# Kernel tuning notes

Hardware: AMD Instinct MI355X
Metric: run time of the kernel (lower is better)

The kernel has to match this reference:

```python
import jax, jax.numpy as jnp
import numpy as np

B, T, D_IN, H, NUM_LAYERS = 64, 512, 512, 500, 2


def _lstm_dir(x, mask, W_ih, W_hh, b, reverse):
    """One unidirectional LSTM over padded batch. x:[B,T,D], mask:[B,T,1] bool.
    AllenNLP AugmentedLstm gate order: input, forget, memory(cell), output."""
    bsz = x.shape[0]
    h_dim = W_hh.shape[1]
    # Precompute all input-side gate projections in one big GEMM: [B,T,4H]
    x_gates = jnp.einsum('btd,gd->btg', x, W_ih) + b

    def step(carry, inp):
        h, c = carry
        gx, m = inp  # gx:[B,4H], m:[B,1]
        gates = gx + h @ W_hh.T
        i, f, g, o = jnp.split(gates, 4, axis=-1)
        i = jax.nn.sigmoid(i)
        f = jax.nn.sigmoid(f)
        g = jnp.tanh(g)
        o = jax.nn.sigmoid(o)
        c_new = f * c + i * g
        h_new = o * jnp.tanh(c_new)
        h = jnp.where(m, h_new, h)
        c = jnp.where(m, c_new, c)
        return (h, c), h * m  # padded positions emit zeros (like pad_packed_sequence)

    init = (jnp.zeros((bsz, h_dim), x.dtype), jnp.zeros((bsz, h_dim), x.dtype))
    xs = (jnp.swapaxes(x_gates, 0, 1), jnp.swapaxes(mask, 0, 1))
    _, ys = jax.lax.scan(step, init, xs, reverse=reverse)
    return jnp.swapaxes(ys, 0, 1)  # [B,T,H]


def _stacked_bilstm(seqs, mask, params):
    x = seqs
    for (Wf_ih, Wf_hh, bf, Wb_ih, Wb_hh, bb) in params:
        fwd = _lstm_dir(x, mask, Wf_ih, Wf_hh, bf, reverse=False)
        bwd = _lstm_dir(x, mask, Wb_ih, Wb_hh, bb, reverse=True)
        x = jnp.concatenate([fwd, bwd], axis=-1)
    return x


def setup_inputs() -> dict:
    key = jax.random.key(0)
    ks = jax.random.split(key, 16)
    seqs = jax.random.normal(ks[0], (B, T, D_IN), dtype=jnp.float32)
    lengths = jnp.clip(jax.random.randint(ks[1], (B,), 0, T + 1), 1, T).astype(jnp.int64)
    inp = {'seqs': seqs, 'lengths': lengths}
    scale = 0.05
    d_in = D_IN
    idx = 2
    for l in range(NUM_LAYERS):
        for d in ('f', 'b'):
            inp[f'W_ih{l}{d}'] = jax.random.normal(ks[idx], (4 * H, d_in), dtype=jnp.float32) * scale; idx += 1
            inp[f'W_hh{l}{d}'] = jax.random.normal(ks[idx], (4 * H, H), dtype=jnp.float32) * scale; idx += 1
            inp[f'b{l}{d}'] = jnp.zeros((4 * H,), dtype=jnp.float32)
        d_in = 2 * H
    return inp


def reference(seqs, lengths, W_ih0f, W_hh0f, b0f, W_ih0b, W_hh0b, b0b,
              W_ih1f, W_hh1f, b1f, W_ih1b, W_hh1b, b1b):
    mask = (jnp.arange(T)[None, :] < lengths[:, None])[..., None]  # [B,T,1] bool
    params = [
        (W_ih0f, W_hh0f, b0f, W_ih0b, W_hh0b, b0b),
        (W_ih1f, W_hh1f, b1f, W_ih1b, W_hh1b, b1b),
    ]
    return _stacked_bilstm(seqs, mask, params)  # [B,T,2H]
```

## Files before the change

kernel.cpp:

```cpp
#include <hip/hip_runtime.h>
#include <cstdint>
#include <cstddef>

#define BB   64
#define TT   512
#define HH   500
#define G4H  2000
#define KPAD 512
#define TCH  64
#define D1P  1024
#define NPAD 2048
#define UPB  16
#define NB2  32
#define WSL2 (32 * 64 * 512)

typedef _Float16 v8h __attribute__((ext_vector_type(8)));
typedef _Float16 v4h __attribute__((ext_vector_type(4)));
typedef float    v4f __attribute__((ext_vector_type(4)));

union F16x8 { unsigned long long u[2]; float4 f4; v8h h; };
union H16B  { _Float16 f; unsigned short u; };

__device__ __forceinline__ float sigm(float x) { return 1.f / (1.f + __expf(-x)); }
__device__ __forceinline__ float tanh_fast(float x) {
    float e = __expf(2.f * x);
    return 1.f - 2.f / (e + 1.f);
}

__device__ __forceinline__ void gload_lds16(const _Float16* src, _Float16* dst) {
    __builtin_amdgcn_global_load_lds(
        (const __attribute__((address_space(1))) void*)src,
        (__attribute__((address_space(3))) void*)dst, 16, 0, 0);
}


__global__ __launch_bounds__(256) void pad_whh16_kernel(
    const float* __restrict__ w0, const float* __restrict__ w1,
    const float* __restrict__ w2, const float* __restrict__ w3,
    _Float16* __restrict__ dst)
{
    int idx = blockIdx.x * 256 + threadIdx.x;
    int k = idx & 511;
    int t = idx >> 9;
    int r = t & 63;  t >>= 6;
    int bi = t & 31;
    int ld = t >> 5;
    int g = r >> 4, j = r & 15;
    int u = bi * UPB + j;
    const float* src = (ld == 0) ? w0 : (ld == 1) ? w1 : (ld == 2) ? w2 : w3;
    float val = (u < HH && k < HH) ? src[(size_t)(g * HH + u) * HH + k] : 0.f;
    dst[idx] = (_Float16)val;
}

__global__ __launch_bounds__(256) void pad_wih16_kernel(
    const float* __restrict__ wf, const float* __restrict__ wb,
    _Float16* __restrict__ dst, int ksrc, int kshift)
{
    int idx = blockIdx.x * 256 + threadIdx.x;
    int kdst = 1 << kshift;
    int k = idx & (kdst - 1);
    int n = (idx >> kshift) & (NPAD - 1);
    int d = idx >> (kshift + 11);
    int bi = n >> 6, r = n & 63, g = r >> 4, j = r & 15;
    int u = bi * UPB + j;
    const float* src = d ? wb : wf;
    float v = (u < HH && k < ksrc) ? src[(size_t)(g * HH + u) * ksrc + k] : 0.f;
    dst[idx] = (_Float16)v;
}

__global__ __launch_bounds__(256) void bias_perm_kernel(
    const float* __restrict__ b0f_, const float* __restrict__ b0b_,
    const float* __restrict__ b1f_, const float* __restrict__ b1b_,
    float* __restrict__ dst)
{
    int idx = blockIdx.x * 256 + threadIdx.x;
    int n = idx & (NPAD - 1);
    int ld = idx >> 11;
    int bi = n >> 6, r = n & 63, g = r >> 4, j = r & 15;
    int u = bi * UPB + j;
    const float* src = (ld == 0) ? b0f_ : (ld == 1) ? b0b_ : (ld == 2) ? b1f_ : b1b_;
    dst[idx] = (u < HH) ? src[g * HH + u] : 0.f;
}

__global__ __launch_bounds__(256) void f32to16x4_kernel(
    const float* __restrict__ src, _Float16* __restrict__ dst)
{
    int idx = blockIdx.x * 256 + threadIdx.x;
    float4 v = ((const float4*)src)[idx];
    v4h o;
    o[0] = (_Float16)v.x; o[1] = (_Float16)v.y;
    o[2] = (_Float16)v.z; o[3] = (_Float16)v.w;
    ((v4h*)dst)[idx] = o;
}

#define BM 128
#define BN 128
#define BKG 64

__device__ __forceinline__ void gemm_body(
    int g, _Float16* smemh,
    const _Float16* __restrict__ A16, int K,
    const _Float16* __restrict__ W16,
    const float* __restrict__ bf_, const float* __restrict__ bb_,
    float* __restrict__ gates, int t0f, int t0b)
{
    const int mtile = g & 31;
    const int ntile = (g >> 5) & 15;
    const int dir   = g >> 9;
    const int t0  = dir ? t0b : t0f;
    const _Float16* W = W16 + (size_t)dir * NPAD * K;
    const float* bias = dir ? bb_ : bf_;
    const int tid  = threadIdx.x;
    const int lane = tid & 63;
    const int wv = __builtin_amdgcn_readfirstlane(tid >> 6);
    const int wm = wv >> 1, wn = wv & 1;

    _Float16* Asm = smemh;
    _Float16* Bsm = smemh + BM * BKG;

    const _Float16* aPtr[4];
    const _Float16* bPtr[4];
    #pragma unroll
    for (int it = 0; it < 4; ++it) {
        const int s = tid + it * 256;
        const int row = s >> 3;
        const int kswz = ((s ^ row) & 7) << 3;
        const int rg = mtile * BM + row;
        const int b = rg >> 6;
        const int t = t0 + (rg & 63);
        aPtr[it] = A16 + (size_t)(b * TT + t) * K + kswz;
        bPtr[it] = W + (size_t)(ntile * BN + row) * K + kswz;
    }

    v4f acc[4][4];
    #pragma unroll
    for (int mt = 0; mt < 4; ++mt)
        #pragma unroll
        for (int nt = 0; nt < 4; ++nt) acc[mt][nt] = (v4f)(0.f);

    for (int k0 = 0; k0 < K; k0 += BKG) {
        #pragma unroll
        for (int it = 0; it < 4; ++it) {
            gload_lds16(aPtr[it] + k0, &Asm[(tid + it * 256) * 8]);
            gload_lds16(bPtr[it] + k0, &Bsm[(tid + it * 256) * 8]);
        }
        __syncthreads();
        #pragma unroll
        for (int kk = 0; kk < 2; ++kk) {
            v8h af[4], bw[4];
            #pragma unroll
            for (int mt = 0; mt < 4; ++mt) {
                const int row = wm * 64 + mt * 16 + (lane & 15);
                const int slot = (kk * 4 + (lane >> 4)) ^ (row & 7);
                af[mt] = *(const v8h*)&Asm[row * BKG + slot * 8];
            }
            #pragma unroll
            for (int nt = 0; nt < 4; ++nt) {
                const int row = wn * 64 + nt * 16 + (lane & 15);
                const int slot = (kk * 4 + (lane >> 4)) ^ (row & 7);
                bw[nt] = *(const v8h*)&Bsm[row * BKG + slot * 8];
            }
            #pragma unroll
            for (int mt = 0; mt < 4; ++mt)
                #pragma unroll
                for (int nt = 0; nt < 4; ++nt)
                    acc[mt][nt] = __builtin_amdgcn_mfma_f32_16x16x32_f16(
                        af[mt], bw[nt], acc[mt][nt], 0, 0, 0);
        }
        __syncthreads();
    }

    float* gout = gates + (size_t)dir * (BB * TCH * NPAD);
    const int colBase = ntile * BN + wn * 64 + (lane & 15);
    const int rowBase = mtile * BM + wm * 64 + ((lane >> 4) * 4);
    #pragma unroll
    for (int nt = 0; nt < 4; ++nt) {
        const int n = colBase + nt * 16;
        const float bv = bias[n];
        #pragma unroll
        for (int mt = 0; mt < 4; ++mt) {
            const int r = rowBase + mt * 16;
            const int b = r >> 6;
            const int tl = r & 63;
            float* gp = gout + (size_t)(b * TCH + tl) * NPAD + n;
            #pragma unroll
            for (int i = 0; i < 4; ++i)
                gp[(size_t)i * NPAD] = acc[mt][nt][i] + bv;
        }
    }
}

__global__ __launch_bounds__(256, 2) void gemm16_kernel(
    const _Float16* __restrict__ A16, int K,
    const _Float16* __restrict__ W16,
    const float* __restrict__ bf_, const float* __restrict__ bb_,
    float* __restrict__ gates, int t0f, int t0b)
{
    __shared__ _Float16 smemg[BM * BKG + BN * BKG];
    gemm_body(blockIdx.x, smemg, A16, K, W16, bf_, bb_, gates, t0f, t0b);
}

__global__ __launch_bounds__(256, 1) void fused_phase_kernel(
    const float*    __restrict__ gates,
    const _Float16* __restrict__ whh16,
    const int*      __restrict__ lengths,
    _Float16* __restrict__ h16,
    float*    __restrict__ cbuf,
    void*     __restrict__ yout, int y_ld, int yF16,
    int s0, int gstep0,
    unsigned int* __restrict__ flags,
    const _Float16* __restrict__ A16, int K,
    const _Float16* __restrict__ W16,
    const float* __restrict__ bfp, const float* __restrict__ bbp,
    float* __restrict__ gatesN, int nt0f, int nt0b, int doGemm)
{
    __shared__ _Float16 smemh[49152];

    if (blockIdx.x >= 64) {
        if (doGemm)
            gemm_body(blockIdx.x - 64, smemh, A16, K, W16, bfp, bbp,
                      gatesN, nt0f, nt0b);
        return;
    }

    const int tid  = threadIdx.x;
    const int dir  = blockIdx.x >> 5;
    const int bi   = blockIdx.x & 31;
    const int u0   = bi * UPB;
    const int lane = tid & 63;
    const int w    = __builtin_amdgcn_readfirstlane(tid >> 6);

    _Float16* Wl = smemh;

    {
        const _Float16* wsrc = whh16 + (size_t)dir * WSL2 + (size_t)bi * 64 * 512;
        #pragma unroll
        for (int it = 0; it < 16; ++it) {
            const int slot = tid + it * 256;
            const int r = slot >> 6, sp = slot & 63;
            gload_lds16(wsrc + (size_t)r * 512 + ((sp ^ (r & 7)) << 3),
                        Wl + slot * 8);
        }
    }

    const int jn = lane & 15;
    const int hi = lane >> 4;
    const bool uval = (u0 + jn) < HH;
    const int b0 = w * 16 + hi * 4;

    int lenv[4];
    float cst[4], hpv[4];
    #pragma unroll
    for (int i = 0; i < 4; ++i) {
        const int b = b0 + i;
        lenv[i] = lengths[b];
        cst[i]  = cbuf[(size_t)(dir * BB + b) * KPAD + u0 + jn];
        hpv[i]  = (float)h16[((size_t)(dir * 2 + 0) * BB + b) * 512 + u0 + jn];
    }

    __syncthreads();

    v8h bfr[4][16];
    #pragma unroll
    for (int g = 0; g < 4; ++g) {
        #pragma unroll
        for (int kt = 0; kt < 16; ++kt) {
            const int r = g * 16 + jn;
            const int sphys = (kt * 4 + hi) ^ (jn & 7);
            F16x8 bf; bf.f4 = *(const float4*)&Wl[r * 512 + sphys * 8];
            bfr[g][kt] = bf.h;
        }
    }

    const float* gb = gates + (size_t)dir * (BB * TCH * NPAD) + bi * 64 + jn;

    float gxv[4][4];
    {
        const int tl0 = dir ? (TCH - 1) : 0;
        #pragma unroll
        for (int i = 0; i < 4; ++i) {
            const float* gp = gb + ((size_t)((b0 + i) * TCH + tl0)) * NPAD;
            #pragma unroll
            for (int g = 0; g < 4; ++g) gxv[g][i] = gp[g * 16];
        }
    }

    for (int sl = 0; sl < TCH; ++sl) {
        const int s   = s0 + sl;
        const int par = s & 1;
        const int t   = dir ? (TT - 1 - s) : s;

        F16x8 av[16];
        {
            const char* hb = (const char*)(h16 + (size_t)(dir * 2 + par) * BB * 512);
            const size_t base = ((size_t)(w * 16 + jn) * 512 + hi * 8) * 2;
            #pragma unroll
            for (int kt = 0; kt < 16; ++kt) {
                const unsigned long long* p =
                    (const unsigned long long*)(hb + base + (size_t)kt * 64);
                av[kt].u[0] = __hip_atomic_load(p,     __ATOMIC_RELAXED, __HIP_MEMORY_SCOPE_AGENT);
                av[kt].u[1] = __hip_atomic_load(p + 1, __ATOMIC_RELAXED, __HIP_MEMORY_SCOPE_AGENT);
            }
        }

        v4f acc[4];
        #pragma unroll
        for (int g = 0; g < 4; ++g) acc[g] = (v4f)(0.f);
        #pragma unroll
        for (int kt = 0; kt < 16; ++kt) {
            #pragma unroll
            for (int g = 0; g < 4; ++g) {
                acc[g] = __builtin_amdgcn_mfma_f32_16x16x32_f16(
                    av[kt].h, bfr[g][kt], acc[g], 0, 0, 0);
            }
        }

        float ysv[4];
        #pragma unroll
        for (int i = 0; i < 4; ++i) {
            const bool msk = (t < lenv[i]);
            const float p0 = acc[0][i] + gxv[0][i];
            const float p1 = acc[1][i] + gxv[1][i];
            const float p2 = acc[2][i] + gxv[2][i];
            const float p3 = acc[3][i] + gxv[3][i];
            const float ig = sigm(p0);
            const float fg = sigm(p1);
            const float gg = tanh_fast(p2);
            const float og = sigm(p3);
            const float cn = fg * cst[i] + ig * gg;
            const float hn = og * tanh_fast(cn);
            cst[i] = msk ? cn : cst[i];
            hpv[i] = msk ? hn : hpv[i];
            ysv[i] = msk ? hn : 0.f;
        }

        if (uval) {
            #pragma unroll
            for (int i = 0; i < 4; ++i) {
                const int b = b0 + i;
                H16B hb16; hb16.f = (_Float16)hpv[i];
                __hip_atomic_store(
                    (unsigned short*)h16 +
                        ((size_t)(dir * 2 + (par ^ 1)) * BB + b) * 512 + u0 + jn,
                    hb16.u, __ATOMIC_RELAXED, __HIP_MEMORY_SCOPE_AGENT);
            }
        }

        __syncthreads();

        const unsigned int tgt = (unsigned int)(gstep0 + sl + 1);
        if (tid == 0)
            __hip_atomic_store(&flags[(dir * NB2 + bi) * 16], tgt,
                               __ATOMIC_RELAXED, __HIP_MEMORY_SCOPE_AGENT);

        if (uval) {
            #pragma unroll
            for (int i = 0; i < 4; ++i) {
                const int b = b0 + i;
                const size_t yoff = ((size_t)b * TT + t) * y_ld + dir * HH + u0 + jn;
                if (yF16) ((_Float16*)yout)[yoff] = (_Float16)ysv[i];
                else      ((float*)yout)[yoff]    = ysv[i];
            }
        }

        float gxn[4][4];
        const bool hasNext = (sl + 1 < TCH);
        if (hasNext) {
            const int tln = dir ? (TCH - 2 - sl) : (sl + 1);
            #pragma unroll
            for (int i = 0; i < 4; ++i) {
                const float* gp = gb + ((size_t)((b0 + i) * TCH + tln)) * NPAD;
                #pragma unroll
                for (int g = 0; g < 4; ++g) gxn[g][i] = gp[g * 16];
            }
        }
        asm volatile("" ::: "memory");

        if (tid < 64) {
            const int fi = lane & 31;
            const unsigned int* fp = flags + (size_t)(dir * NB2 + fi) * 16;
            for (;;) {
                unsigned int v = __hip_atomic_load(fp, __ATOMIC_RELAXED,
                                                   __HIP_MEMORY_SCOPE_AGENT);
                if (__all(v >= tgt)) break;
                __builtin_amdgcn_s_sleep(1);
            }
        }
        __syncthreads();

        if (hasNext) {
            #pragma unroll
            for (int g = 0; g < 4; ++g)
                #pragma unroll
                for (int i = 0; i < 4; ++i) gxv[g][i] = gxn[g][i];
        }
    }

    if (uval) {
        #pragma unroll
        for (int i = 0; i < 4; ++i)
            cbuf[(size_t)(dir * BB + b0 + i) * KPAD + u0 + jn] = cst[i];
    }
}

extern "C" void kernel_launch(void* const* d_in, const int* in_sizes, int n_in,
                              void* d_out, int out_size, void* d_ws, size_t ws_size,
                              hipStream_t stream)
{
    (void)in_sizes; (void)n_in; (void)out_size; (void)ws_size;

    const float* seqs    = (const float*)d_in[0];
    const int*   lengths = (const int*)  d_in[1];
    const float* W_ih0f  = (const float*)d_in[2];
    const float* W_hh0f  = (const float*)d_in[3];
    const float* b0f     = (const float*)d_in[4];
    const float* W_ih0b  = (const float*)d_in[5];
    const float* W_hh0b  = (const float*)d_in[6];
    const float* b0b     = (const float*)d_in[7];
    const float* W_ih1f  = (const float*)d_in[8];
    const float* W_hh1f  = (const float*)d_in[9];
    const float* b1f     = (const float*)d_in[10];
    const float* W_ih1b  = (const float*)d_in[11];
    const float* W_hh1b  = (const float*)d_in[12];
    const float* b1b     = (const float*)d_in[13];

    char* ws = (char*)d_ws;
    const size_t SZ_GATES = (size_t)2 * BB * TCH * NPAD * 4;
    const size_t SZ_SEQ16 = (size_t)BB * TT * 512 * 2;
    const size_t SZ_OUT16 = (size_t)BB * TT * D1P * 2;
    const size_t SZ_WIH0  = (size_t)2 * NPAD * 512 * 2;
    const size_t SZ_WIH1  = (size_t)2 * NPAD * D1P * 2;
    const size_t SZ_WHH16 = (size_t)4 * WSL2 * 2;
    const size_t SZ_BPERM = (size_t)4 * NPAD * 4;
    const size_t SZ_H16   = (size_t)2 * 2 * BB * 512 * 2;
    const size_t SZ_CBUF  = (size_t)2 * BB * KPAD * 4;
    const size_t SZ_FLAGS = (size_t)64 * 16 * 4;

    size_t off = 0;
    float*     gatesA = (float*)(ws + off);     off += SZ_GATES;
    float*     gatesB = (float*)(ws + off);     off += SZ_GATES;
    _Float16*  seq16  = (_Float16*)(ws + off);  off += SZ_SEQ16;
    _Float16*  out16  = (_Float16*)(ws + off);  off += SZ_OUT16;
    _Float16*  wih016 = (_Float16*)(ws + off);  off += SZ_WIH0;
    _Float16*  wih116 = (_Float16*)(ws + off);  off += SZ_WIH1;
    _Float16*  whh16  = (_Float16*)(ws + off);  off += SZ_WHH16;
    float*     bperm  = (float*)(ws + off);     off += SZ_BPERM;
    _Float16*  h16    = (_Float16*)(ws + off);  off += SZ_H16;
    float*     cbuf   = (float*)(ws + off);     off += SZ_CBUF;
    unsigned int* flags = (unsigned int*)(ws + off);  off += SZ_FLAGS;

    pad_whh16_kernel<<<16384, 256, 0, stream>>>(W_hh0f, W_hh0b, W_hh1f, W_hh1b, whh16);
    pad_wih16_kernel<<<8192,  256, 0, stream>>>(W_ih0f, W_ih0b, wih016, 512, 9);
    pad_wih16_kernel<<<16384, 256, 0, stream>>>(W_ih1f, W_ih1b, wih116, 1000, 10);
    bias_perm_kernel<<<32,    256, 0, stream>>>(b0f, b0b, b1f, b1b, bperm);
    f32to16x4_kernel<<<16384, 256, 0, stream>>>(seqs, seq16);
    hipMemsetAsync(out16, 0, SZ_OUT16, stream);
    hipMemsetAsync(flags, 0, SZ_FLAGS, stream);

    for (int layer = 0; layer < 2; ++layer) {
        hipMemsetAsync(h16, 0, SZ_H16, stream);
        hipMemsetAsync(cbuf, 0, SZ_CBUF, stream);

        const _Float16* A16  = layer ? out16 : seq16;
        const int       K    = layer ? D1P : 512;
        const _Float16* WL   = layer ? wih116 : wih016;
        const float*    bfp  = bperm + (size_t)(layer * 2 + 0) * NPAD;
        const float*    bbp  = bperm + (size_t)(layer * 2 + 1) * NPAD;
        const _Float16* whhL = whh16 + (size_t)layer * 2 * WSL2;
        void*           yo   = layer ? d_out : (void*)out16;
        const int       y_ld = layer ? 1000 : D1P;
        const int       yF16 = layer ? 0 : 1;

        gemm16_kernel<<<1024, 256, 0, stream>>>(
            A16, K, WL, bfp, bbp, gatesA, 0, TT - TCH);

        for (int ph = 0; ph < 8; ++ph) {
            float* gcur = (ph & 1) ? gatesB : gatesA;
            float* gnxt = (ph & 1) ? gatesA : gatesB;
            const int doG  = (ph < 7) ? 1 : 0;
            const int nt0f = (ph + 1) * TCH;
            const int nt0b = TT - TCH * (ph + 2);
            const int gstep0 = layer * TT + ph * TCH;
            fused_phase_kernel<<<doG ? 1088 : 64, 256, 0, stream>>>(
                gcur, whhL, lengths, h16, cbuf, yo, y_ld, yF16,
                ph * TCH, gstep0, flags,
                A16, K, WL, bfp, bbp, gnxt, nt0f, nt0b, doG);
        }
    }
}
```

Before: 6.524 ms.

## Halve recurrent blocks to 16 per direction with 32 hidden units each

Each recurrent workgroup now owns 32 hidden units instead of 16, so each direction uses 16 blocks rather than 32. Every wave covers a 32-batch by 16-unit tile using two MFMA row tiles. The change roughly halves the number of flags each block polls at every timestep, which should cut cross-block synchronisation cost on the serial path. It also drops the LDS staging of W_hh in favour of direct global loads into registers, and removes the prefetch of the next step's gate inputs, so those loads now sit on the critical path and each block does twice the per-step MFMA and activation work.

```diff
diff --git a/kernel.cpp b/kernel.cpp
--- a/kernel.cpp
+++ b/kernel.cpp
@@ -10,9 +10,9 @@
 #define TCH  64
 #define D1P  1024
 #define NPAD 2048
-#define UPB  16
-#define NB2  32
-#define WSL2 (32 * 64 * 512)
+#define UPB  32
+#define NB2  16
+#define WSL2 (16 * 128 * 512)
 
 typedef _Float16 v8h __attribute__((ext_vector_type(8)));
 typedef _Float16 v4h __attribute__((ext_vector_type(4)));
@@ -42,10 +42,10 @@
     int idx = blockIdx.x * 256 + threadIdx.x;
     int k = idx & 511;
     int t = idx >> 9;
-    int r = t & 63;  t >>= 6;
-    int bi = t & 31;
-    int ld = t >> 5;
-    int g = r >> 4, j = r & 15;
+    int r = t & 127;  t >>= 7;
+    int bi = t & 15;
+    int ld = t >> 4;
+    int g = r >> 5, j = r & 31;
     int u = bi * UPB + j;
     const float* src = (ld == 0) ? w0 : (ld == 1) ? w1 : (ld == 2) ? w2 : w3;
     float val = (u < HH && k < HH) ? src[(size_t)(g * HH + u) * HH + k] : 0.f;
@@ -61,7 +61,7 @@
     int k = idx & (kdst - 1);
     int n = (idx >> kshift) & (NPAD - 1);
     int d = idx >> (kshift + 11);
-    int bi = n >> 6, r = n & 63, g = r >> 4, j = r & 15;
+    int bi = n >> 7, r = n & 127, g = r >> 5, j = r & 31;
     int u = bi * UPB + j;
     const float* src = d ? wb : wf;
     float v = (u < HH && k < ksrc) ? src[(size_t)(g * HH + u) * ksrc + k] : 0.f;
@@ -76,7 +76,7 @@
     int idx = blockIdx.x * 256 + threadIdx.x;
     int n = idx & (NPAD - 1);
     int ld = idx >> 11;
-    int bi = n >> 6, r = n & 63, g = r >> 4, j = r & 15;
+    int bi = n >> 7, r = n & 127, g = r >> 5, j = r & 31;
     int u = bi * UPB + j;
     const float* src = (ld == 0) ? b0f_ : (ld == 1) ? b0b_ : (ld == 2) ? b1f_ : b1b_;
     dst[idx] = (u < HH) ? src[g * HH + u] : 0.f;
@@ -216,133 +216,150 @@
 {
     __shared__ _Float16 smemh[49152];
 
-    if (blockIdx.x >= 64) {
+    if (blockIdx.x >= 32) {
         if (doGemm)
-            gemm_body(blockIdx.x - 64, smemh, A16, K, W16, bfp, bbp,
+            gemm_body(blockIdx.x - 32, smemh, A16, K, W16, bfp, bbp,
                       gatesN, nt0f, nt0b);
         return;
     }
 
     const int tid  = threadIdx.x;
-    const int dir  = blockIdx.x >> 5;
-    const int bi   = blockIdx.x & 31;
+    const int dir  = blockIdx.x >> 4;
+    const int bi   = blockIdx.x & 15;
     const int u0   = bi * UPB;
     const int lane = tid & 63;
-    const int w    = __builtin_amdgcn_readfirstlane(tid >> 6);
-
-    _Float16* Wl = smemh;
-
+    const int wv   = __builtin_amdgcn_readfirstlane(tid >> 6);
+    const int bh   = wv >> 1;
+    const int jh   = wv & 1;
+    const int c    = lane & 15;
+    const int hi   = lane >> 4;
+    const int j    = jh * 16 + c;
+    const int u    = u0 + j;
+    const bool uval = (u < HH);
+
+    v8h bfr[4][16];
     {
-        const _Float16* wsrc = whh16 + (size_t)dir * WSL2 + (size_t)bi * 64 * 512;
-        #pragma unroll
-        for (int it = 0; it < 16; ++it) {
-            const int slot = tid + it * 256;
-            const int r = slot >> 6, sp = slot & 63;
-            gload_lds16(wsrc + (size_t)r * 512 + ((sp ^ (r & 7)) << 3),
-                        Wl + slot * 8);
-        }
-    }
-
-    const int jn = lane & 15;
-    const int hi = lane >> 4;
-    const bool uval = (u0 + jn) < HH;
-    const int b0 = w * 16 + hi * 4;
-
-    int lenv[4];
-    float cst[4], hpv[4];
+        const _Float16* wblk = whh16 + (size_t)dir * WSL2 + (size_t)bi * 128 * 512;
+        #pragma unroll
+        for (int g = 0; g < 4; ++g) {
+            #pragma unroll
+            for (int kt = 0; kt < 16; ++kt) {
+                F16x8 f;
+                f.f4 = *(const float4*)(wblk + (size_t)(g * 32 + j) * 512
+                                        + kt * 32 + hi * 8);
+                bfr[g][kt] = f.h;
+            }
+        }
+    }
+
+    int lenv[8];
+    float cst[8], hpv[8];
     #pragma unroll
-    for (int i = 0; i < 4; ++i) {
-        const int b = b0 + i;
-        lenv[i] = lengths[b];
-        cst[i]  = cbuf[(size_t)(dir * BB + b) * KPAD + u0 + jn];
-        hpv[i]  = (float)h16[((size_t)(dir * 2 + 0) * BB + b) * 512 + u0 + jn];
+    for (int mt = 0; mt < 2; ++mt) {
+        #pragma unroll
+        for (int i = 0; i < 4; ++i) {
+            const int idx = mt * 4 + i;
+            const int b = bh * 32 + mt * 16 + hi * 4 + i;
+            lenv[idx] = lengths[b];
+            cst[idx]  = cbuf[(size_t)(dir * BB + b) * KPAD + u];
+            hpv[idx]  = (float)h16[((size_t)(dir * 2 + 0) * BB + b) * 512 + u];
+        }
     }
 
     __syncthreads();
 
-    v8h bfr[4][16];
-    #pragma unroll
-    for (int g = 0; g < 4; ++g) {
-        #pragma unroll
-        for (int kt = 0; kt < 16; ++kt) {
-            const int r = g * 16 + jn;
-            const int sphys = (kt * 4 + hi) ^ (jn & 7);
-            F16x8 bf; bf.f4 = *(const float4*)&Wl[r * 512 + sphys * 8];
-            bfr[g][kt] = bf.h;
-        }
-    }
-
-    const float* gb = gates + (size_t)dir * (BB * TCH * NPAD) + bi * 64 + jn;
-
-    float gxv[4][4];
-    {
-        const int tl0 = dir ? (TCH - 1) : 0;
-        #pragma unroll
-        for (int i = 0; i < 4; ++i) {
-            const float* gp = gb + ((size_t)((b0 + i) * TCH + tl0)) * NPAD;
-            #pragma unroll
-            for (int g = 0; g < 4; ++g) gxv[g][i] = gp[g * 16];
-        }
-    }
+    const float* gb = gates + (size_t)dir * (BB * TCH * NPAD) + bi * 128 + j;
 
     for (int sl = 0; sl < TCH; ++sl) {
         const int s   = s0 + sl;
         const int par = s & 1;
         const int t   = dir ? (TT - 1 - s) : s;
-
-        F16x8 av[16];
+        const int tl  = dir ? (TCH - 1 - sl) : sl;
+
+        F16x8 av[2][16];
         {
             const char* hb = (const char*)(h16 + (size_t)(dir * 2 + par) * BB * 512);
-            const size_t base = ((size_t)(w * 16 + jn) * 512 + hi * 8) * 2;
-            #pragma unroll
-            for (int kt = 0; kt < 16; ++kt) {
-                const unsigned long long* p =
-                    (const unsigned long long*)(hb + base + (size_t)kt * 64);
-                av[kt].u[0] = __hip_atomic_load(p,     __ATOMIC_RELAXED, __HIP_MEMORY_SCOPE_AGENT);
-                av[kt].u[1] = __hip_atomic_load(p + 1, __ATOMIC_RELAXED, __HIP_MEMORY_SCOPE_AGENT);
-            }
-        }
-
-        v4f acc[4];
-        #pragma unroll
-        for (int g = 0; g < 4; ++g) acc[g] = (v4f)(0.f);
+            #pragma unroll
+            for (int mt = 0; mt < 2; ++mt) {
+                const size_t base = ((size_t)(bh * 32 + mt * 16 + c) * 512 + hi * 8) * 2;
+                #pragma unroll
+                for (int kt = 0; kt < 16; ++kt) {
+                    const unsigned long long* p =
+                        (const unsigned long long*)(hb + base + (size_t)kt * 64);
+                    av[mt][kt].u[0] = __hip_atomic_load(p,     __ATOMIC_RELAXED, __HIP_MEMORY_SCOPE_AGENT);
+                    av[mt][kt].u[1] = __hip_atomic_load(p + 1, __ATOMIC_RELAXED, __HIP_MEMORY_SCOPE_AGENT);
+                }
+            }
+        }
+
+        float gxv[8][4];
+        #pragma unroll
+        for (int mt = 0; mt < 2; ++mt) {
+            #pragma unroll
+            for (int i = 0; i < 4; ++i) {
+                const int b = bh * 32 + mt * 16 + hi * 4 + i;
+                const float* gp = gb + ((size_t)(b * TCH + tl)) * NPAD;
+                #pragma unroll
+                for (int g = 0; g < 4; ++g) gxv[mt * 4 + i][g] = gp[g * 32];
+            }
+        }
+
+        v4f acc[2][4];
+        #pragma unroll
+        for (int mt = 0; mt < 2; ++mt)
+            #pragma unroll
+            for (int g = 0; g < 4; ++g) acc[mt][g] = (v4f)(0.f);
         #pragma unroll
         for (int kt = 0; kt < 16; ++kt) {
             #pragma unroll
-            for (int g = 0; g < 4; ++g) {
-                acc[g] = __builtin_amdgcn_mfma_f32_16x16x32_f16(
-                    av[kt].h, bfr[g][kt], acc[g], 0, 0, 0);
-            }
-        }
-
-        float ysv[4];
-        #pragma unroll
-        for (int i = 0; i < 4; ++i) {
-            const bool msk = (t < lenv[i]);
-            const float p0 = acc[0][i] + gxv[0][i];
-            const float p1 = acc[1][i] + gxv[1][i];
-            const float p2 = acc[2][i] + gxv[2][i];
-            const float p3 = acc[3][i] + gxv[3][i];
-            const float ig = sigm(p0);
-            const float fg = sigm(p1);
-            const float gg = tanh_fast(p2);
-            const float og = sigm(p3);
-            const float cn = fg * cst[i] + ig * gg;
-            const float hn = og * tanh_fast(cn);
-            cst[i] = msk ? cn : cst[i];
-            hpv[i] = msk ? hn : hpv[i];
-            ysv[i] = msk ? hn : 0.f;
+            for (int mt = 0; mt < 2; ++mt) {
+                #pragma unroll
+                for (int g = 0; g < 4; ++g) {
+                    acc[mt][g] = __builtin_amdgcn_mfma_f32_16x16x32_f16(
+                        av[mt][kt].h, bfr[g][kt], acc[mt][g], 0, 0, 0);
+                }
+            }
+        }
+
+        float ysv[8];
+        #pragma unroll
+        for (int mt = 0; mt < 2; ++mt) {
+            #pragma unroll
+            for (int i = 0; i < 4; ++i) {
+                const int idx = mt * 4 + i;
+                const bool msk = (t < lenv[idx]);
+                const float p0 = acc[mt][0][i] + gxv[idx][0];
+                const float p1 = acc[mt][1][i] + gxv[idx][1];
+                const float p2 = acc[mt][2][i] + gxv[idx][2];
+                const float p3 = acc[mt][3][i] + gxv[idx][3];
+                const float ig = sigm(p0);
+                const float fg = sigm(p1);
+                const float gg = tanh_fast(p2);
+                const float og = sigm(p3);
+                const float cn = fg * cst[idx] + ig * gg;
+                const float hn = og * tanh_fast(cn);
+                cst[idx] = msk ? cn : cst[idx];
+                hpv[idx] = msk ? hn : hpv[idx];
+                ysv[idx] = msk ? hn : 0.f;
+            }
         }
 
         if (uval) {
             #pragma unroll
-            for (int i = 0; i < 4; ++i) {
-                const int b = b0 + i;
-                H16B hb16; hb16.f = (_Float16)hpv[i];
-                __hip_atomic_store(
-                    (unsigned short*)h16 +
-                        ((size_t)(dir * 2 + (par ^ 1)) * BB + b) * 512 + u0 + jn,
-                    hb16.u, __ATOMIC_RELAXED, __HIP_MEMORY_SCOPE_AGENT);
+            for (int mt = 0; mt < 2; ++mt) {
+                #pragma unroll
+                for (int i = 0; i < 4; ++i) {
+                    const int idx = mt * 4 + i;
+                    const int b = bh * 32 + mt * 16 + hi * 4 + i;
+                    H16B hb16; hb16.f = (_Float16)hpv[idx];
+                    __hip_atomic_store(
+                        (unsigned short*)h16 +
+                            ((size_t)(dir * 2 + (par ^ 1)) * BB + b) * 512 + u,
+                        hb16.u, __ATOMIC_RELAXED, __HIP_MEMORY_SCOPE_AGENT);
+                    const size_t yoff = ((size_t)b * TT + t) * y_ld + dir * HH + u;
+                    if (yF16) ((_Float16*)yout)[yoff] = (_Float16)ysv[idx];
+                    else      ((float*)yout)[yoff]    = ysv[idx];
+                }
             }
         }
 
@@ -353,31 +370,8 @@
             __hip_atomic_store(&flags[(dir * NB2 + bi) * 16], tgt,
                                __ATOMIC_RELAXED, __HIP_MEMORY_SCOPE_AGENT);
 
-        if (uval) {
-            #pragma unroll
-            for (int i = 0; i < 4; ++i) {
-                const int b = b0 + i;
-                const size_t yoff = ((size_t)b * TT + t) * y_ld + dir * HH + u0 + jn;
-                if (yF16) ((_Float16*)yout)[yoff] = (_Float16)ysv[i];
-                else      ((float*)yout)[yoff]    = ysv[i];
-            }
-        }
-
-        float gxn[4][4];
-        const bool hasNext = (sl + 1 < TCH);
-        if (hasNext) {
-            const int tln = dir ? (TCH - 2 - sl) : (sl + 1);
-            #pragma unroll
-            for (int i = 0; i < 4; ++i) {
-                const float* gp = gb + ((size_t)((b0 + i) * TCH + tln)) * NPAD;
-                #pragma unroll
-                for (int g = 0; g < 4; ++g) gxn[g][i] = gp[g * 16];
-            }
-        }
-        asm volatile("" ::: "memory");
-
         if (tid < 64) {
-            const int fi = lane & 31;
+            const int fi = lane & 15;
             const unsigned int* fp = flags + (size_t)(dir * NB2 + fi) * 16;
             for (;;) {
                 unsigned int v = __hip_atomic_load(fp, __ATOMIC_RELAXED,
@@ -387,19 +381,17 @@
             }
         }
         __syncthreads();
-
-        if (hasNext) {
-            #pragma unroll
-            for (int g = 0; g < 4; ++g)
-                #pragma unroll
-                for (int i = 0; i < 4; ++i) gxv[g][i] = gxn[g][i];
-        }
     }
 
     if (uval) {
         #pragma unroll
-        for (int i = 0; i < 4; ++i)
-            cbuf[(size_t)(dir * BB + b0 + i) * KPAD + u0 + jn] = cst[i];
+        for (int mt = 0; mt < 2; ++mt) {
+            #pragma unroll
+            for (int i = 0; i < 4; ++i) {
+                const int b = bh * 32 + mt * 16 + hi * 4 + i;
+                cbuf[(size_t)(dir * BB + b) * KPAD + u] = cst[mt * 4 + i];
+            }
+        }
     }
 }
 
@@ -481,7 +473,7 @@
             const int nt0f = (ph + 1) * TCH;
             const int nt0b = TT - TCH * (ph + 2);
             const int gstep0 = layer * TT + ph * TCH;
-            fused_phase_kernel<<<doG ? 1088 : 64, 256, 0, stream>>>(
+            fused_phase_kernel<<<doG ? 1056 : 32, 256, 0, stream>>>(
                 gcur, whhL, lengths, h16, cbuf, yo, y_ld, yF16,
                 ph * TCH, gstep0, flags,
                 A16, K, WL, bfp, bbp, gnxt, nt0f, nt0b, doG);
```

Measured after the change: 12.52 ms. 1.92x slower.
